# Optimization experiments

Hardware: AMD Instinct MI355X
Metric: run time of the kernel (lower is better)

Reference implementation:

```python
import jax, jax.numpy as jnp
import numpy as np

N_NODES = 10000
N_REL = 500
H = 128
L = 128
EPS = 1e-12  # matches torch F.normalize eps


def _l2_normalize(x):
    # F.normalize(x, 2, -1): x / max(||x||_2, eps)
    n = jnp.sqrt(jnp.sum(x * x, axis=-1, keepdims=True))
    return x / jnp.maximum(n, EPS)


def setup_inputs() -> dict:
    key = jax.random.key(0)
    k1, k2, k3, k4 = jax.random.split(key, 4)
    return {
        "node_emb": jax.random.normal(k1, (N_NODES, H), dtype=jnp.float32),
        "rel_emb": jax.random.normal(k2, (N_REL, H), dtype=jnp.float32),
        "ent_idxs": jax.random.randint(k3, (L,), 0, N_NODES, dtype=jnp.int64 if jax.config.jax_enable_x64 else jnp.int32),
        "rel_idxs": jax.random.randint(k4, (L,), 0, N_REL, dtype=jnp.int64 if jax.config.jax_enable_x64 else jnp.int32),
    }


def reference(node_emb, rel_emb, ent_idxs, rel_idxs):
    # gather + L2 normalize  (TransE head+rel query vs all normalized entities)
    sel_ent = _l2_normalize(node_emb[ent_idxs])   # [L, H]
    sel_rel = _l2_normalize(rel_emb[rel_idxs])    # [L, H]
    all_ent = _l2_normalize(node_emb)             # [N, H]
    query = sel_ent + sel_rel                     # [L, H]
    # broadcasted difference instead of .repeat(): [L, N, H]
    diff = query[:, None, :] - all_ent[None, :, :]
    dist = jnp.sum(jnp.abs(diff), axis=-1)        # p_norm = 1 -> [L, N]
    # loss_name == 'BCELoss' -> softmax over all entities
    return jax.nn.softmax(dist, axis=-1)
```

## Files before the change

### kernel.cpp

```cpp
#include <hip/hip_runtime.h>
#include <math.h>

#define N_NODES 10000
#define N_REL   500
#define H       128
#define L       128

#define TL 32
#define TN 64
#define HC 64
#define NB 157

__device__ __forceinline__ float waveReduceSum(float v) {
    #pragma unroll
    for (int m = 1; m < 64; m <<= 1) v += __shfl_xor(v, m, 64);
    return v;
}

__global__ __launch_bounds__(256) void k_prep(const float* __restrict__ node,
                                              const float* __restrict__ rel,
                                              const int* __restrict__ eidx,
                                              const int* __restrict__ ridx,
                                              float* __restrict__ invn,
                                              float* __restrict__ query) {
    int wave = threadIdx.x >> 6;
    int lane = threadIdx.x & 63;
    if (blockIdx.x < 2500) {
        int row = blockIdx.x * 4 + wave;
        float2 v = *reinterpret_cast<const float2*>(node + row * H + lane * 2);
        float ss = waveReduceSum(v.x * v.x + v.y * v.y);
        if (lane == 0) invn[row] = 1.0f / fmaxf(sqrtf(ss), 1e-12f);
    } else {
        int l = (blockIdx.x - 2500) * 4 + wave;
        int ei = eidx[l], ri = ridx[l];
        float2 e = *reinterpret_cast<const float2*>(node + ei * H + lane * 2);
        float inve = 1.0f / fmaxf(sqrtf(waveReduceSum(e.x * e.x + e.y * e.y)), 1e-12f);
        float2 r = *reinterpret_cast<const float2*>(rel + ri * H + lane * 2);
        float invr = 1.0f / fmaxf(sqrtf(waveReduceSum(r.x * r.x + r.y * r.y)), 1e-12f);
        float2 q;
        q.x = e.x * inve + r.x * invr;
        q.y = e.y * inve + r.y * invr;
        *reinterpret_cast<float2*>(query + l * H + lane * 2) = q;
    }
}

__global__ __launch_bounds__(256) void k_dist(const float* __restrict__ node,
                                              const float* __restrict__ invn,
                                              const float* __restrict__ query,
                                              float* __restrict__ out,
                                              float* __restrict__ pmax,
                                              float* __restrict__ psum) {
    __shared__ float qs[HC * TL];
    __shared__ float es[HC * TN];

    int nb = blockIdx.x * TN;
    int lb = blockIdx.y * TL;
    int tid = threadIdx.x;
    int tl = tid >> 4;
    int tn = tid & 15;

    float acc[2][4] = {};

    for (int hb = 0; hb < H; hb += HC) {
        #pragma unroll
        for (int k = 0; k < 2; ++k) {
            int f  = tid + (k << 8);
            int r  = f >> 4;
            int c4 = (f & 15) << 2;
            float4 v = *reinterpret_cast<const float4*>(query + (lb + r) * H + hb + c4);
            int rs = r ^ (c4 & 28);
            qs[(c4 + 0) * TL + rs] = v.x;
            qs[(c4 + 1) * TL + rs] = v.y;
            qs[(c4 + 2) * TL + rs] = v.z;
            qs[(c4 + 3) * TL + rs] = v.w;
        }
        #pragma unroll
        for (int k = 0; k < 4; ++k) {
            int f  = tid + (k << 8);
            int r  = f >> 4;
            int c4 = (f & 15) << 2;
            int gn = nb + r;
            float4 v = make_float4(0.f, 0.f, 0.f, 0.f);
            float s = 0.f;
            if (gn < N_NODES) {
                v = *reinterpret_cast<const float4*>(node + gn * H + hb + c4);
                s = invn[gn];
            }
            int rs = r ^ (c4 & 60);
            es[(c4 + 0) * TN + rs] = v.x * s;
            es[(c4 + 1) * TN + rs] = v.y * s;
            es[(c4 + 2) * TN + rs] = v.z * s;
            es[(c4 + 3) * TN + rs] = v.w * s;
        }
        __syncthreads();

        #pragma unroll
        for (int h = 0; h < HC; ++h) {
            float2 q2 = *reinterpret_cast<const float2*>(&qs[h * TL + ((tl << 1) ^ (h & 28))]);
            float4 e4 = *reinterpret_cast<const float4*>(&es[h * TN + ((tn << 2) ^ (h & 60))]);
            float qa[2] = {q2.x, q2.y};
            float ea[4] = {e4.x, e4.y, e4.z, e4.w};
            #pragma unroll
            for (int i = 0; i < 2; ++i)
                #pragma unroll
                for (int j = 0; j < 4; ++j)
                    acc[i][j] += fabsf(qa[i] - ea[j]);
        }
        __syncthreads();
    }

    int n0 = nb + (tn << 2);
    bool valid = n0 < N_NODES;

    float rmax[2], rsum[2];
    #pragma unroll
    for (int i = 0; i < 2; ++i) {
        float m = valid ? fmaxf(fmaxf(acc[i][0], acc[i][1]), fmaxf(acc[i][2], acc[i][3]))
                        : -INFINITY;
        #pragma unroll
        for (int s = 1; s < 16; s <<= 1) m = fmaxf(m, __shfl_xor(m, s, 64));
        rmax[i] = m;
        float p[4], sum = 0.f;
        #pragma unroll
        for (int j = 0; j < 4; ++j) {
            p[j] = valid ? expf(acc[i][j] - m) : 0.f;
            sum += p[j];
        }
        #pragma unroll
        for (int s = 1; s < 16; s <<= 1) sum += __shfl_xor(sum, s, 64);
        rsum[i] = sum;
        if (valid) {
            int l = lb + (tl << 1) + i;
            *reinterpret_cast<float4*>(out + (size_t)l * N_NODES + n0) =
                make_float4(p[0], p[1], p[2], p[3]);
        }
    }
    if (tn == 0) {
        #pragma unroll
        for (int i = 0; i < 2; ++i) {
            int l = lb + (tl << 1) + i;
            pmax[l * NB + blockIdx.x] = rmax[i];
            psum[l * NB + blockIdx.x] = rsum[i];
        }
    }
}

__global__ __launch_bounds__(256) void k_finish(float* __restrict__ out,
                                                const float* __restrict__ pmax,
                                                const float* __restrict__ psum) {
    __shared__ float red[8];
    int l = blockIdx.y;
    int tid = threadIdx.x;
    const float* pm = pmax + l * NB;
    const float* ps = psum + l * NB;

    float m = (tid < NB) ? pm[tid] : -INFINITY;
    #pragma unroll
    for (int s = 1; s < 64; s <<= 1) m = fmaxf(m, __shfl_xor(m, s, 64));
    if ((tid & 63) == 0) red[tid >> 6] = m;
    __syncthreads();
    float gmax = fmaxf(fmaxf(red[0], red[1]), fmaxf(red[2], red[3]));

    float sum = (tid < NB) ? ps[tid] * expf(pm[tid] - gmax) : 0.f;
    #pragma unroll
    for (int s = 1; s < 64; s <<= 1) sum += __shfl_xor(sum, s, 64);
    if ((tid & 63) == 0) red[4 + (tid >> 6)] = sum;
    __syncthreads();
    float inv = 1.0f / (red[4] + red[5] + red[6] + red[7]);

    int n4 = blockIdx.x * 256 + tid;
    if (n4 < 2500) {
        int blk = n4 >> 4;
        float f = expf(pm[blk] - gmax) * inv;
        float4* o = reinterpret_cast<float4*>(out) + (size_t)l * 2500 + n4;
        float4 v = *o;
        v.x *= f; v.y *= f; v.z *= f; v.w *= f;
        *o = v;
    }
}

extern "C" void kernel_launch(void* const* d_in, const int* in_sizes, int n_in,
                              void* d_out, int out_size, void* d_ws, size_t ws_size,
                              hipStream_t stream) {
    const float* node = (const float*)d_in[0];
    const float* rel  = (const float*)d_in[1];
    const int*   eidx = (const int*)d_in[2];
    const int*   ridx = (const int*)d_in[3];
    float* out = (float*)d_out;

    float* invn  = (float*)d_ws;
    float* query = (float*)d_ws + 10240;
    float* pmax  = (float*)d_ws + 26624;
    float* psum  = (float*)d_ws + 46720;

    k_prep<<<2532, 256, 0, stream>>>(node, rel, eidx, ridx, invn, query);

    dim3 gridB(NB, L / TL);
    k_dist<<<gridB, 256, 0, stream>>>(node, invn, query, out, pmax, psum);

    dim3 gridD((2500 + 255) / 256, L);
    k_finish<<<gridD, 256, 0, stream>>>(out, pmax, psum);
}
```

Baseline: 31.73 us.

## Retile distance kernel with direct-to-LDS loads and drop softmax max pass

The distance kernel now loads the full 128-wide hidden dimension for an 80-node by 64-query tile in one pass. It uses global_load_lds to write straight into XOR-swizzled shared memory, then scales the entity rows by their inverse norms in place. Each thread computes a 4x5 register tile with float4 reads. The softmax max-subtraction is removed: the L1 distance between normalized vectors is bounded (about 34), so exp cannot overflow, and the pmax buffer and its finish-kernel pass go away. In exchange the grid drops to 250 large blocks with about 81 KB of LDS each, which leaves at most one block per CU and less latency hiding.

```diff
diff --git a/kernel.cpp b/kernel.cpp
--- a/kernel.cpp
+++ b/kernel.cpp
@@ -6,15 +6,20 @@
 #define H       128
 #define L       128
 
-#define TL 32
-#define TN 64
-#define HC 64
-#define NB 157
+#define TN   80
+#define TL   64
+#define NBX  125
+#define PADF 2100
 
 __device__ __forceinline__ float waveReduceSum(float v) {
     #pragma unroll
     for (int m = 1; m < 64; m <<= 1) v += __shfl_xor(v, m, 64);
     return v;
+}
+
+__device__ __forceinline__ void gload16(const float* g, float* l) {
+    __builtin_amdgcn_global_load_lds((const __attribute__((address_space(1))) void*)g,
+                                     (__attribute__((address_space(3))) void*)l, 16, 0, 0);
 }
 
 __global__ __launch_bounds__(256) void k_prep(const float* __restrict__ node,
@@ -48,133 +53,112 @@
                                               const float* __restrict__ invn,
                                               const float* __restrict__ query,
                                               float* __restrict__ out,
-                                              float* __restrict__ pmax,
                                               float* __restrict__ psum) {
-    __shared__ float qs[HC * TL];
-    __shared__ float es[HC * TN];
+    __shared__ float es[TN * H + PADF];
+    __shared__ float qs[TL * H];
+    __shared__ float invs[TN];
 
-    int nb = blockIdx.x * TN;
-    int lb = blockIdx.y * TL;
-    int tid = threadIdx.x;
-    int tl = tid >> 4;
-    int tn = tid & 15;
+    const int tid  = threadIdx.x;
+    const int wav  = tid >> 6;
+    const int lane = tid & 63;
+    const int nb   = blockIdx.x * TN;
+    const int lb   = blockIdx.y * TL;
 
-    float acc[2][4] = {};
+    if (tid < TN) invs[tid] = invn[nb + tid];
 
-    for (int hb = 0; hb < H; hb += HC) {
+    {
+        const int rl = lane >> 5;
+        const int c0 = (lane & 31) << 2;
         #pragma unroll
-        for (int k = 0; k < 2; ++k) {
-            int f  = tid + (k << 8);
-            int r  = f >> 4;
-            int c4 = (f & 15) << 2;
-            float4 v = *reinterpret_cast<const float4*>(query + (lb + r) * H + hb + c4);
-            int rs = r ^ (c4 & 28);
-            qs[(c4 + 0) * TL + rs] = v.x;
-            qs[(c4 + 1) * TL + rs] = v.y;
-            qs[(c4 + 2) * TL + rs] = v.z;
-            qs[(c4 + 3) * TL + rs] = v.w;
+        for (int k = 0; k < 10; ++k) {
+            int row = wav * 20 + k * 2 + rl;
+            int g = ((row >> 2) & 7) << 2;
+            gload16(node + (size_t)(nb + row) * H + (c0 ^ g),
+                    &es[(wav * 20 + k * 2) * H]);
         }
         #pragma unroll
-        for (int k = 0; k < 4; ++k) {
-            int f  = tid + (k << 8);
-            int r  = f >> 4;
-            int c4 = (f & 15) << 2;
-            int gn = nb + r;
-            float4 v = make_float4(0.f, 0.f, 0.f, 0.f);
-            float s = 0.f;
-            if (gn < N_NODES) {
-                v = *reinterpret_cast<const float4*>(node + gn * H + hb + c4);
-                s = invn[gn];
-            }
-            int rs = r ^ (c4 & 60);
-            es[(c4 + 0) * TN + rs] = v.x * s;
-            es[(c4 + 1) * TN + rs] = v.y * s;
-            es[(c4 + 2) * TN + rs] = v.z * s;
-            es[(c4 + 3) * TN + rs] = v.w * s;
+        for (int k = 0; k < 8; ++k) {
+            int row = wav * 16 + k * 2 + rl;
+            int g = ((row >> 2) & 7) << 2;
+            gload16(query + (size_t)(lb + row) * H + (c0 ^ g),
+                    &qs[(wav * 16 + k * 2) * H]);
         }
-        __syncthreads();
+    }
+    __syncthreads();
 
+    #pragma unroll
+    for (int k = 0; k < 10; ++k) {
+        int d4 = tid + (k << 8);
+        float s = invs[d4 >> 5];
+        float4* p = reinterpret_cast<float4*>(es) + d4;
+        float4 v = *p;
+        v.x *= s; v.y *= s; v.z *= s; v.w *= s;
+        *p = v;
+    }
+    __syncthreads();
+
+    const int tl = tid >> 4;
+    const int tn = tid & 15;
+    const int l0 = tl * 4;
+    const int n0 = tn * 5;
+    const int gq = (tl & 7) << 2;
+    int ge[5];
+    #pragma unroll
+    for (int j = 0; j < 5; ++j) ge[j] = (((n0 + j) >> 2) & 7) << 2;
+
+    float acc[4][5] = {};
+
+    #pragma unroll 4
+    for (int h4 = 0; h4 < 32; ++h4) {
+        const int h = h4 << 2;
+        float4 qf[4], ef[5];
         #pragma unroll
-        for (int h = 0; h < HC; ++h) {
-            float2 q2 = *reinterpret_cast<const float2*>(&qs[h * TL + ((tl << 1) ^ (h & 28))]);
-            float4 e4 = *reinterpret_cast<const float4*>(&es[h * TN + ((tn << 2) ^ (h & 60))]);
-            float qa[2] = {q2.x, q2.y};
-            float ea[4] = {e4.x, e4.y, e4.z, e4.w};
+        for (int i = 0; i < 4; ++i)
+            qf[i] = *reinterpret_cast<const float4*>(&qs[(l0 + i) * H + (h ^ gq)]);
+        #pragma unroll
+        for (int j = 0; j < 5; ++j)
+            ef[j] = *reinterpret_cast<const float4*>(&es[(n0 + j) * H + (h ^ ge[j])]);
+        #pragma unroll
+        for (int i = 0; i < 4; ++i)
             #pragma unroll
-            for (int i = 0; i < 2; ++i)
-                #pragma unroll
-                for (int j = 0; j < 4; ++j)
-                    acc[i][j] += fabsf(qa[i] - ea[j]);
-        }
-        __syncthreads();
+            for (int j = 0; j < 5; ++j)
+                acc[i][j] += fabsf(qf[i].x - ef[j].x) + fabsf(qf[i].y - ef[j].y)
+                           + fabsf(qf[i].z - ef[j].z) + fabsf(qf[i].w - ef[j].w);
     }
 
-    int n0 = nb + (tn << 2);
-    bool valid = n0 < N_NODES;
-
-    float rmax[2], rsum[2];
     #pragma unroll
-    for (int i = 0; i < 2; ++i) {
-        float m = valid ? fmaxf(fmaxf(acc[i][0], acc[i][1]), fmaxf(acc[i][2], acc[i][3]))
-                        : -INFINITY;
+    for (int i = 0; i < 4; ++i) {
+        int l = lb + l0 + i;
+        float rs = 0.f;
         #pragma unroll
-        for (int s = 1; s < 16; s <<= 1) m = fmaxf(m, __shfl_xor(m, s, 64));
-        rmax[i] = m;
-        float p[4], sum = 0.f;
-        #pragma unroll
-        for (int j = 0; j < 4; ++j) {
-            p[j] = valid ? expf(acc[i][j] - m) : 0.f;
-            sum += p[j];
+        for (int j = 0; j < 5; ++j) {
+            float p = expf(acc[i][j]);
+            rs += p;
+            out[(size_t)l * N_NODES + nb + n0 + j] = p;
         }
         #pragma unroll
-        for (int s = 1; s < 16; s <<= 1) sum += __shfl_xor(sum, s, 64);
-        rsum[i] = sum;
-        if (valid) {
-            int l = lb + (tl << 1) + i;
-            *reinterpret_cast<float4*>(out + (size_t)l * N_NODES + n0) =
-                make_float4(p[0], p[1], p[2], p[3]);
-        }
-    }
-    if (tn == 0) {
-        #pragma unroll
-        for (int i = 0; i < 2; ++i) {
-            int l = lb + (tl << 1) + i;
-            pmax[l * NB + blockIdx.x] = rmax[i];
-            psum[l * NB + blockIdx.x] = rsum[i];
-        }
+        for (int s = 1; s < 16; s <<= 1) rs += __shfl_xor(rs, s, 64);
+        if (tn == 0) psum[l * NBX + blockIdx.x] = rs;
     }
 }
 
 __global__ __launch_bounds__(256) void k_finish(float* __restrict__ out,
-                                                const float* __restrict__ pmax,
                                                 const float* __restrict__ psum) {
-    __shared__ float red[8];
+    __shared__ float red[4];
     int l = blockIdx.y;
     int tid = threadIdx.x;
-    const float* pm = pmax + l * NB;
-    const float* ps = psum + l * NB;
-
-    float m = (tid < NB) ? pm[tid] : -INFINITY;
+    float s = (tid < NBX) ? psum[l * NBX + tid] : 0.f;
     #pragma unroll
-    for (int s = 1; s < 64; s <<= 1) m = fmaxf(m, __shfl_xor(m, s, 64));
-    if ((tid & 63) == 0) red[tid >> 6] = m;
+    for (int m = 1; m < 64; m <<= 1) s += __shfl_xor(s, m, 64);
+    if ((tid & 63) == 0) red[tid >> 6] = s;
     __syncthreads();
-    float gmax = fmaxf(fmaxf(red[0], red[1]), fmaxf(red[2], red[3]));
-
-    float sum = (tid < NB) ? ps[tid] * expf(pm[tid] - gmax) : 0.f;
-    #pragma unroll
-    for (int s = 1; s < 64; s <<= 1) sum += __shfl_xor(sum, s, 64);
-    if ((tid & 63) == 0) red[4 + (tid >> 6)] = sum;
-    __syncthreads();
-    float inv = 1.0f / (red[4] + red[5] + red[6] + red[7]);
+    float inv = 1.0f / (red[0] + red[1] + red[2] + red[3]);
 
     int n4 = blockIdx.x * 256 + tid;
     if (n4 < 2500) {
-        int blk = n4 >> 4;
-        float f = expf(pm[blk] - gmax) * inv;
         float4* o = reinterpret_cast<float4*>(out) + (size_t)l * 2500 + n4;
         float4 v = *o;
-        v.x *= f; v.y *= f; v.z *= f; v.w *= f;
+        v.x *= inv; v.y *= inv; v.z *= inv; v.w *= inv;
         *o = v;
     }
 }
@@ -190,14 +174,13 @@
 
     float* invn  = (float*)d_ws;
     float* query = (float*)d_ws + 10240;
-    float* pmax  = (float*)d_ws + 26624;
-    float* psum  = (float*)d_ws + 46720;
+    float* psum  = (float*)d_ws + 26624;
 
     k_prep<<<2532, 256, 0, stream>>>(node, rel, eidx, ridx, invn, query);
 
-    dim3 gridB(NB, L / TL);
-    k_dist<<<gridB, 256, 0, stream>>>(node, invn, query, out, pmax, psum);
+    dim3 gridB(NBX, L / TL);
+    k_dist<<<gridB, 256, 0, stream>>>(node, invn, query, out, psum);
 
-    dim3 gridD((2500 + 255) / 256, L);
-    k_finish<<<gridD, 256, 0, stream>>>(out, pmax, psum);
+    dim3 gridC((2500 + 255) / 256, L);
+    k_finish<<<gridC, 256, 0, stream>>>(out, psum);
 }
```

New measurement: 35.25 us. 1.11x slower.
